# Optimization experiments

Hardware: AMD Instinct MI355X
Metric: run time of the kernel (lower is better)

Reference implementation:

```python
import jax, jax.numpy as jnp
import numpy as np

D_MODEL = 1024
N_HEAD = 16
D_K = 64
D_V = 64
LN_EPS = 1e-5


def setup_inputs() -> dict:
    key = jax.random.key(0)
    ks = jax.random.split(key, 12)
    B, S = 4, 2048
    s = 1.0 / np.sqrt(D_MODEL)
    inp = {
        "q": jax.random.normal(ks[0], (B, S, D_MODEL), jnp.float32),
        "k": jax.random.normal(ks[1], (B, S, D_MODEL), jnp.float32),
        "v": jax.random.normal(ks[2], (B, S, D_MODEL), jnp.float32),
        "mask": jnp.ones((B, S, S), jnp.int32),
        "w_q": jax.random.normal(ks[3], (D_MODEL, N_HEAD * D_K), jnp.float32) * s,
        "b_q": jnp.zeros((N_HEAD * D_K,), jnp.float32),
        "w_k": jax.random.normal(ks[4], (D_MODEL, N_HEAD * D_K), jnp.float32) * s,
        "b_k": jnp.zeros((N_HEAD * D_K,), jnp.float32),
        "w_v": jax.random.normal(ks[5], (D_MODEL, N_HEAD * D_V), jnp.float32) * s,
        "b_v": jnp.zeros((N_HEAD * D_V,), jnp.float32),
        "w_fc": jax.random.normal(ks[6], (N_HEAD * D_V, D_MODEL), jnp.float32) * s,
        "b_fc": jnp.zeros((D_MODEL,), jnp.float32),
        "ln_g": jnp.ones((D_MODEL,), jnp.float32),
        "ln_b": jnp.zeros((D_MODEL,), jnp.float32),
    }
    return inp


def reference(q, k, v, mask, w_q, b_q, w_k, b_k, w_v, b_v, w_fc, b_fc, ln_g, ln_b):
    B, Sq, _ = q.shape
    Sk = k.shape[1]
    residual = q
    # QKV projections -> [B, H, S, d]
    qh = (q @ w_q + b_q).reshape(B, Sq, N_HEAD, D_K).transpose(0, 2, 1, 3)
    kh = (k @ w_k + b_k).reshape(B, Sk, N_HEAD, D_K).transpose(0, 2, 1, 3)
    vh = (v @ w_v + b_v).reshape(B, Sk, N_HEAD, D_V).transpose(0, 2, 1, 3)
    temp = jnp.sqrt(jnp.asarray(D_K, qh.dtype))
    scores = jnp.einsum("bhqd,bhkd->bhqk", qh / temp, kh)
    scores = jnp.where(mask[:, None, :, :] == 0, jnp.asarray(-1e9, scores.dtype), scores)
    attn = jax.nn.softmax(scores, axis=-1)  # dropout is identity in eval
    out = jnp.einsum("bhqk,bhkd->bhqd", attn, vh)
    out = out.transpose(0, 2, 1, 3).reshape(B, Sq, N_HEAD * D_V)
    out = out @ w_fc + b_fc  # output proj (dropout identity)
    x = out + residual
    mu = jnp.mean(x, axis=-1, keepdims=True)
    var = jnp.mean(jnp.square(x - mu), axis=-1, keepdims=True)
    y = (x - mu) * jax.lax.rsqrt(var + LN_EPS) * ln_g + ln_b
    return (y, attn)
```

## Files before the change

### kernel.cpp

```cpp
#include <hip/hip_runtime.h>
#include <cstdint>
#include <cstddef>

#define DM 1024
#define HN 16
#define DH 64
#define BB 4
#define SS 2048
#define MM (BB * SS)

typedef __bf16 bf16;
typedef bf16 bf16x8 __attribute__((ext_vector_type(8)));
typedef bf16 bf16x4 __attribute__((ext_vector_type(4)));
typedef float f32x4 __attribute__((ext_vector_type(4)));

__device__ __forceinline__ f32x4 mfma16(bf16x8 a, bf16x8 b, f32x4 c) {
  return __builtin_amdgcn_mfma_f32_16x16x32_bf16(a, b, c, 0, 0, 0);
}

typedef __attribute__((address_space(3))) void lds_void_t;
typedef __attribute__((address_space(1))) void glob_void_t;

__device__ __forceinline__ void gload16(const void* g, void* l) {
  __builtin_amdgcn_global_load_lds((const glob_void_t*)g, (lds_void_t*)l, 16, 0, 0);
}

__global__ __launch_bounds__(256) void mask_bits(const int* __restrict__ mask,
                                                 unsigned long long* __restrict__ mbits) {
  size_t i = (size_t)blockIdx.x * 256 + threadIdx.x;
  int m = mask[i];
  unsigned long long w = __ballot(m != 0);
  if ((threadIdx.x & 63) == 0) mbits[i >> 6] = w;
}

__global__ __launch_bounds__(256) void cvt3(const float* __restrict__ q,
                                            const float* __restrict__ k,
                                            const float* __restrict__ v,
                                            bf16* __restrict__ dst) {
  int which = blockIdx.y;
  const float* in = which == 0 ? q : which == 1 ? k : v;
  bf16* out = dst + (size_t)which * MM * DM;
  int i = (blockIdx.x * 256 + threadIdx.x) * 8;
  f32x4 a = *(const f32x4*)(in + i);
  f32x4 b = *(const f32x4*)(in + i + 4);
  bf16x8 o;
  o[0] = (bf16)a[0]; o[1] = (bf16)a[1]; o[2] = (bf16)a[2]; o[3] = (bf16)a[3];
  o[4] = (bf16)b[0]; o[5] = (bf16)b[1]; o[6] = (bf16)b[2]; o[7] = (bf16)b[3];
  *(bf16x8*)(out + i) = o;
}

__global__ __launch_bounds__(256) void wtrans4(const float* __restrict__ w_q,
                                               const float* __restrict__ w_k,
                                               const float* __restrict__ w_v,
                                               const float* __restrict__ w_fc,
                                               bf16* __restrict__ WT) {
  int p = blockIdx.z;
  const float* W = p == 0 ? w_q : p == 1 ? w_k : p == 2 ? w_v : w_fc;
  bf16* out = WT + (size_t)p * DM * DM;
  __shared__ float t[32][33];
  int n0 = blockIdx.x * 32, k0 = blockIdx.y * 32;
  int tid = threadIdx.x;
  int r = tid >> 3, c = (tid & 7) * 4;
  f32x4 v = *(const f32x4*)&W[(size_t)(k0 + r) * DM + n0 + c];
  t[r][c] = v[0]; t[r][c + 1] = v[1]; t[r][c + 2] = v[2]; t[r][c + 3] = v[3];
  __syncthreads();
  bf16x4 o;
#pragma unroll
  for (int i = 0; i < 4; ++i) o[i] = (bf16)t[c + i][r];
  *(bf16x4*)&out[(size_t)(n0 + r) * DM + k0 + c] = o;
}

__global__ __launch_bounds__(256) void gemm_qkv(const bf16* __restrict__ Abase,
                                                const bf16* __restrict__ Bt,
                                                const float* __restrict__ b_q,
                                                const float* __restrict__ b_k,
                                                const float* __restrict__ b_v,
                                                bf16* __restrict__ qhh,
                                                bf16* __restrict__ khh,
                                                bf16* __restrict__ vhT) {
  constexpr int K = DM;
  __shared__ bf16 Ab[128 * 32];
  __shared__ bf16 Bb[128 * 32];
  int tid = threadIdx.x, wave = tid >> 6, lane = tid & 63;
  int bm = blockIdx.x * 128, bn = blockIdx.y * 128;
  int proj = bn >> 10;
  const bf16* A = Abase + (size_t)proj * MM * DM;
  const float* bias = proj == 0 ? b_q : proj == 1 ? b_k : b_v;
  int wr = (wave >> 1) * 64, wc = (wave & 1) * 64;
  int fr = lane & 15, kg8 = (lane >> 4) * 8;
  f32x4 acc[4][4] = {};
  int arow = tid >> 2, acol = (tid & 3) * 8;
  const bf16* Ag0 = A + (size_t)(bm + arow) * K + acol;
  const bf16* Ag1 = Ag0 + (size_t)64 * K;
  const bf16* Bg0 = Bt + (size_t)(bn + arow) * K + acol;
  const bf16* Bg1 = Bg0 + (size_t)64 * K;
  char* la = (char*)Ab + wave * 1024;
  char* lb = (char*)Bb + wave * 1024;
  for (int k0 = 0; k0 < K; k0 += 32) {
    __syncthreads();
    gload16(Ag0 + k0, la);
    gload16(Ag1 + k0, la + 4096);
    gload16(Bg0 + k0, lb);
    gload16(Bg1 + k0, lb + 4096);
    asm volatile("s_waitcnt vmcnt(0)" ::: "memory");
    __syncthreads();
    bf16x8 af[4], bfr[4];
#pragma unroll
    for (int m = 0; m < 4; ++m)
      af[m] = *(const bf16x8*)&Ab[(wr + m * 16 + fr) * 32 + kg8];
#pragma unroll
    for (int n = 0; n < 4; ++n)
      bfr[n] = *(const bf16x8*)&Bb[(wc + n * 16 + fr) * 32 + kg8];
#pragma unroll
    for (int m = 0; m < 4; ++m)
#pragma unroll
      for (int n = 0; n < 4; ++n) acc[m][n] = mfma16(af[m], bfr[n], acc[m][n]);
  }
  int b = bm >> 11;
#pragma unroll
  for (int m = 0; m < 4; ++m)
#pragma unroll
    for (int n = 0; n < 4; ++n) {
      int c = bn + wc + n * 16 + fr;
      int lc = c & 1023;
      float bv = bias[lc];
      int h = lc >> 6, d = lc & 63;
      int r0 = bm + wr + m * 16 + (lane >> 4) * 4;
      int s0 = r0 & (SS - 1);
      if (proj == 2) {
        bf16x4 o;
#pragma unroll
        for (int j = 0; j < 4; ++j) o[j] = (bf16)(acc[m][n][j] + bv);
        *(bf16x4*)&vhT[(size_t)(b * HN + h) * (SS * DH) +
                       (size_t)(s0 >> 5) * (DH * 32) + d * 32 + (s0 & 31)] = o;
      } else {
        bf16* dst = proj == 0 ? qhh : khh;
        float sc = proj == 0 ? 0.125f : 1.f;
#pragma unroll
        for (int j = 0; j < 4; ++j) {
          float v = (acc[m][n][j] + bv) * sc;
          dst[(size_t)(b * HN + h) * (SS * DH) + (size_t)(s0 + j) * DH + d] =
              (bf16)v;
        }
      }
    }
}

__global__ __launch_bounds__(256) void gemm_out(const bf16* __restrict__ A,
                                                const bf16* __restrict__ Bt,
                                                const float* __restrict__ bias,
                                                const float* __restrict__ resid,
                                                float* __restrict__ out) {
  constexpr int K = DM;
  __shared__ bf16 Ab[128 * 32];
  __shared__ bf16 Bb[128 * 32];
  int tid = threadIdx.x, wave = tid >> 6, lane = tid & 63;
  int bm = blockIdx.x * 128, bn = blockIdx.y * 128;
  int wr = (wave >> 1) * 64, wc = (wave & 1) * 64;
  int fr = lane & 15, kg8 = (lane >> 4) * 8;
  f32x4 acc[4][4] = {};
  int arow = tid >> 2, acol = (tid & 3) * 8;
  const bf16* Ag0 = A + (size_t)(bm + arow) * K + acol;
  const bf16* Ag1 = Ag0 + (size_t)64 * K;
  const bf16* Bg0 = Bt + (size_t)(bn + arow) * K + acol;
  const bf16* Bg1 = Bg0 + (size_t)64 * K;
  char* la = (char*)Ab + wave * 1024;
  char* lb = (char*)Bb + wave * 1024;
  for (int k0 = 0; k0 < K; k0 += 32) {
    __syncthreads();
    gload16(Ag0 + k0, la);
    gload16(Ag1 + k0, la + 4096);
    gload16(Bg0 + k0, lb);
    gload16(Bg1 + k0, lb + 4096);
    asm volatile("s_waitcnt vmcnt(0)" ::: "memory");
    __syncthreads();
    bf16x8 af[4], bfr[4];
#pragma unroll
    for (int m = 0; m < 4; ++m)
      af[m] = *(const bf16x8*)&Ab[(wr + m * 16 + fr) * 32 + kg8];
#pragma unroll
    for (int n = 0; n < 4; ++n)
      bfr[n] = *(const bf16x8*)&Bb[(wc + n * 16 + fr) * 32 + kg8];
#pragma unroll
    for (int m = 0; m < 4; ++m)
#pragma unroll
      for (int n = 0; n < 4; ++n) acc[m][n] = mfma16(af[m], bfr[n], acc[m][n]);
  }
#pragma unroll
  for (int m = 0; m < 4; ++m)
#pragma unroll
    for (int n = 0; n < 4; ++n) {
      int c = bn + wc + n * 16 + fr;
      float bv = bias[c];
#pragma unroll
      for (int j = 0; j < 4; ++j) {
        int r = bm + wr + m * 16 + (lane >> 4) * 4 + j;
        size_t idx = (size_t)r * DM + c;
        out[idx] = acc[m][n][j] + bv + resid[idx];
      }
    }
}

__global__ __launch_bounds__(1024, 4) void attn_kernel(
    const bf16* __restrict__ qh, const bf16* __restrict__ kh,
    const bf16* __restrict__ vhT, const unsigned int* __restrict__ mbits,
    float* __restrict__ attn_out, bf16* __restrict__ ctx) {
  extern __shared__ char smem[];
  float* pbuf = (float*)(smem + 32 * 4096);
  float* invp = (float*)(smem + 32 * 4096 + 8192);
  int tid = threadIdx.x, wave = tid >> 6, lane = tid & 63;
  int fid = (blockIdx.x & 7) * 512 + (blockIdx.x >> 3);
  int bh = fid >> 6, qt = fid & 63;
  int b = bh >> 4, h = bh & 15;
  int q0 = qt * 32;
  const bf16* qbase = qh + ((size_t)bh * SS + q0) * DH;
  const bf16* kbase = kh + (size_t)bh * SS * DH;
  const bf16* vbase = vhT + (size_t)bh * SS * DH;
  int fr = lane & 15, kg = lane >> 4;

  bf16x8 qa0 = *(const bf16x8*)&qbase[(size_t)fr * DH + kg * 8];
  bf16x8 qa1 = *(const bf16x8*)&qbase[(size_t)fr * DH + 32 + kg * 8];
  bf16x8 qb0 = *(const bf16x8*)&qbase[(size_t)(16 + fr) * DH + kg * 8];
  bf16x8 qb1 = *(const bf16x8*)&qbase[(size_t)(16 + fr) * DH + 32 + kg * 8];

  {
    int sw = wave * 128;
    bf16x8 kb0[8], kb1[8];
    auto kload = [&](int g) {
      const bf16* kp = kbase + (size_t)(sw + g * 16 + fr) * DH + kg * 8;
      kb0[g & 7] = *(const bf16x8*)kp;
      kb1[g & 7] = *(const bf16x8*)(kp + 32);
    };
#pragma unroll
    for (int g = 0; g < 4; ++g) kload(g);
#pragma unroll
    for (int g = 0; g < 8; ++g) {
      if (g < 4) kload(g + 4);
      f32x4 aa = {0.f, 0.f, 0.f, 0.f};
      f32x4 ab = {0.f, 0.f, 0.f, 0.f};
      aa = mfma16(qa0, kb0[g & 7], aa);
      aa = mfma16(qa1, kb1[g & 7], aa);
      ab = mfma16(qb0, kb0[g & 7], ab);
      ab = mfma16(qb1, kb1[g & 7], ab);
      int col = sw + g * 16 + fr;
      int slot = col >> 3, within = col & 7;
#pragma unroll
      for (int j = 0; j < 4; ++j) {
        int ra = kg * 4 + j;
        int rb = ra + 16;
        *(bf16*)(smem + ra * 4096 + ((slot ^ ra) << 4) + within * 2) =
            (bf16)aa[j];
        *(bf16*)(smem + rb * 4096 + ((slot ^ rb) << 4) + within * 2) =
            (bf16)ab[j];
      }
    }
  }
  __syncthreads();

  {
    int row = wave * 2 + (lane >> 5);
    int la = lane & 31;
    char* rbase = smem + row * 4096;
    const unsigned int* mrow32 = mbits + ((size_t)b * SS + q0 + row) * 64;
    float sum = 0.f;
#pragma unroll
    for (int it = 0; it < 8; ++it) {
      int slot = la + it * 32;
      char* p = rbase + ((slot ^ row) << 4);
      bf16x8 e = *(const bf16x8*)p;
      unsigned int bits = mrow32[slot >> 2] >> ((slot & 3) * 8);
      bf16x8 w8;
#pragma unroll
      for (int i = 0; i < 8; ++i) {
        float f = __expf((float)e[i]);
        f = ((bits >> i) & 1u) ? f : 0.f;
        sum += f;
        w8[i] = (bf16)f;
      }
      *(bf16x8*)p = w8;
    }
#pragma unroll
    for (int off = 1; off < 32; off <<= 1) sum += __shfl_xor(sum, off);
    if (la == 0) invp[row] = 1.f / sum;
  }
  __syncthreads();

  {
    int t = tid & 511, rh = tid >> 9;
    int slot = t >> 1, halfoff = (t & 1) * 8;
    float* outb = attn_out + ((size_t)bh * SS + q0) * SS;
#pragma unroll
    for (int it = 0; it < 16; ++it) {
      int r = it * 2 + rh;
      bf16x4 e = *(const bf16x4*)(smem + r * 4096 + ((slot ^ r) << 4) + halfoff);
      float inv = invp[r];
      f32x4 u = {(float)e[0] * inv, (float)e[1] * inv, (float)e[2] * inv,
                 (float)e[3] * inv};
      *(f32x4*)(outb + (size_t)r * SS + t * 4) = u;
    }
  }

  {
    int rb = wave >> 3, dq = (wave >> 1) & 3, kh2 = wave & 1;
    f32x4 cacc = {0.f, 0.f, 0.f, 0.f};
    const bf16* vtile = vbase + (size_t)(kh2 * 32) * (DH * 32) +
                        (dq * 16 + fr) * 32 + kg * 8;
    int prow_row = rb * 16 + fr;
    char* prow = smem + prow_row * 4096;
    bf16x8 vb[8], pb[8];
    auto pvload = [&](int kk) {
      vb[kk & 7] = *(const bf16x8*)&vtile[(size_t)kk * (DH * 32)];
      int slotA = kh2 * 128 + kk * 4 + kg;
      pb[kk & 7] = *(const bf16x8*)(prow + ((slotA ^ prow_row) << 4));
    };
    pvload(0);
    pvload(1);
    pvload(2);
    pvload(3);
#pragma unroll
    for (int kk = 0; kk < 32; ++kk) {
      if (kk < 28) pvload(kk + 4);
      cacc = mfma16(pb[kk & 7], vb[kk & 7], cacc);
    }
    if (kh2 == 1) {
#pragma unroll
      for (int j = 0; j < 4; ++j)
        pbuf[((rb * 4 + dq) * 16 + kg * 4 + j) * 16 + fr] = cacc[j];
    }
    __syncthreads();
    if (kh2 == 0) {
#pragma unroll
      for (int j = 0; j < 4; ++j) {
        int row = rb * 16 + kg * 4 + j;
        float v = (cacc[j] + pbuf[((rb * 4 + dq) * 16 + kg * 4 + j) * 16 + fr]) *
                  invp[row];
        ctx[((size_t)b * SS + q0 + row) * DM + h * DH + dq * 16 + fr] = (bf16)v;
      }
    }
  }
}

__global__ __launch_bounds__(256) void ln_k(float* __restrict__ x,
                                            const float* __restrict__ g,
                                            const float* __restrict__ bln) {
  int r = blockIdx.x, tid = threadIdx.x;
  f32x4 v = *(const f32x4*)&x[(size_t)r * DM + tid * 4];
  float s = v[0] + v[1] + v[2] + v[3];
  float s2 = v[0] * v[0] + v[1] * v[1] + v[2] * v[2] + v[3] * v[3];
#pragma unroll
  for (int off = 32; off; off >>= 1) {
    s += __shfl_down(s, off);
    s2 += __shfl_down(s2, off);
  }
  __shared__ float rs_[4], rs2_[4];
  int wave = tid >> 6, lane = tid & 63;
  if (lane == 0) {
    rs_[wave] = s;
    rs2_[wave] = s2;
  }
  __syncthreads();
  s = rs_[0] + rs_[1] + rs_[2] + rs_[3];
  s2 = rs2_[0] + rs2_[1] + rs2_[2] + rs2_[3];
  float mu = s * (1.f / DM);
  float var = s2 * (1.f / DM) - mu * mu;
  float rstd = rsqrtf(var + 1e-5f);
  f32x4 gg = *(const f32x4*)&g[tid * 4];
  f32x4 bb = *(const f32x4*)&bln[tid * 4];
  f32x4 o;
#pragma unroll
  for (int i = 0; i < 4; ++i) o[i] = (v[i] - mu) * rstd * gg[i] + bb[i];
  *(f32x4*)&x[(size_t)r * DM + tid * 4] = o;
}

extern "C" void kernel_launch(void* const* d_in, const int* in_sizes, int n_in,
                              void* d_out, int out_size, void* d_ws,
                              size_t ws_size, hipStream_t stream) {
  const float* q = (const float*)d_in[0];
  const float* k = (const float*)d_in[1];
  const float* v = (const float*)d_in[2];
  const int* mask = (const int*)d_in[3];
  const float* w_q = (const float*)d_in[4];
  const float* b_q = (const float*)d_in[5];
  const float* w_k = (const float*)d_in[6];
  const float* b_k = (const float*)d_in[7];
  const float* w_v = (const float*)d_in[8];
  const float* b_v = (const float*)d_in[9];
  const float* w_fc = (const float*)d_in[10];
  const float* b_fc = (const float*)d_in[11];
  const float* ln_g = (const float*)d_in[12];
  const float* ln_b = (const float*)d_in[13];

  float* y = (float*)d_out;
  float* attn_out = (float*)d_out + (size_t)MM * DM;

  char* w = (char*)d_ws;
  const size_t actN = (size_t)MM * DM;
  bf16* qkv_bf = (bf16*)w;  w += 3 * actN * 2;
  bf16* wT = (bf16*)w;      w += (size_t)4 * DM * DM * 2;
  bf16* qhh = (bf16*)w;     w += actN * 2;
  bf16* khh = (bf16*)w;     w += actN * 2;
  bf16* vhT = (bf16*)w;     w += actN * 2;
  bf16* ctx = (bf16*)w;     w += actN * 2;
  unsigned long long* mb = (unsigned long long*)w;  w += (size_t)BB * SS * SS / 8;

  mask_bits<<<(BB * SS * SS) / 256, 256, 0, stream>>>(mask, mb);
  cvt3<<<dim3(4096, 3), 256, 0, stream>>>(q, k, v, qkv_bf);
  wtrans4<<<dim3(DM / 32, DM / 32, 4), 256, 0, stream>>>(w_q, w_k, w_v, w_fc, wT);
  gemm_qkv<<<dim3(MM / 128, 3072 / 128), 256, 0, stream>>>(
      qkv_bf, wT, b_q, b_k, b_v, qhh, khh, vhT);
  hipFuncSetAttribute((const void*)attn_kernel,
                      hipFuncAttributeMaxDynamicSharedMemorySize, 139392);
  attn_kernel<<<4096, 1024, 139392, stream>>>(
      qhh, khh, vhT, (const unsigned int*)mb, attn_out, ctx);
  gemm_out<<<dim3(MM / 128, DM / 128), 256, 0, stream>>>(
      ctx, wT + (size_t)3 * DM * DM, b_fc, q, y);
  ln_k<<<MM, 256, 0, stream>>>(y, ln_g, ln_b);
}
```

Before: 671.1 us.

## Fuse exp and mask into score epilogue, transpose mask bits, move attn store last

The mask is repacked into a column-major bitmask (one 32-bit word per key column per 32-query tile), so the QK^T epilogue can apply exp and the mask directly from registers before writing to LDS. The softmax pass then only sums the row, with no read-modify-write of LDS. The full attention-probability store is moved after the PV product, so that store can overlap or trail the matmul work. The new mask kernel has each thread loop over 32 rows with strided loads, which may coalesce less well than the old ballot-based packer.

```diff
diff --git a/kernel.cpp b/kernel.cpp
--- a/kernel.cpp
+++ b/kernel.cpp
@@ -13,6 +13,7 @@
 typedef bf16 bf16x8 __attribute__((ext_vector_type(8)));
 typedef bf16 bf16x4 __attribute__((ext_vector_type(4)));
 typedef float f32x4 __attribute__((ext_vector_type(4)));
+typedef int i32x4 __attribute__((ext_vector_type(4)));
 
 __device__ __forceinline__ f32x4 mfma16(bf16x8 a, bf16x8 b, f32x4 c) {
   return __builtin_amdgcn_mfma_f32_16x16x32_bf16(a, b, c, 0, 0, 0);
@@ -25,12 +26,24 @@
   __builtin_amdgcn_global_load_lds((const glob_void_t*)g, (lds_void_t*)l, 16, 0, 0);
 }
 
-__global__ __launch_bounds__(256) void mask_bits(const int* __restrict__ mask,
-                                                 unsigned long long* __restrict__ mbits) {
-  size_t i = (size_t)blockIdx.x * 256 + threadIdx.x;
-  int m = mask[i];
-  unsigned long long w = __ballot(m != 0);
-  if ((threadIdx.x & 63) == 0) mbits[i >> 6] = w;
+__global__ __launch_bounds__(256) void mask_bitsT(const int* __restrict__ mask,
+                                                  unsigned int* __restrict__ mT) {
+  int qt = blockIdx.x, b = blockIdx.y;
+  int col0 = threadIdx.x * 8;
+  unsigned int m[8] = {0, 0, 0, 0, 0, 0, 0, 0};
+  const int* mp = mask + ((size_t)b * SS + qt * 32) * SS + col0;
+  for (int r = 0; r < 32; ++r) {
+    i32x4 a = *(const i32x4*)(mp + (size_t)r * SS);
+    i32x4 c = *(const i32x4*)(mp + (size_t)r * SS + 4);
+#pragma unroll
+    for (int i = 0; i < 4; ++i) {
+      m[i] |= (unsigned int)(a[i] != 0) << r;
+      m[4 + i] |= (unsigned int)(c[i] != 0) << r;
+    }
+  }
+#pragma unroll
+  for (int i = 0; i < 8; ++i)
+    mT[((size_t)b * 64 + qt) * SS + col0 + i] = m[i];
 }
 
 __global__ __launch_bounds__(256) void cvt3(const float* __restrict__ q,
@@ -203,7 +216,7 @@
 
 __global__ __launch_bounds__(1024, 4) void attn_kernel(
     const bf16* __restrict__ qh, const bf16* __restrict__ kh,
-    const bf16* __restrict__ vhT, const unsigned int* __restrict__ mbits,
+    const bf16* __restrict__ vhT, const unsigned int* __restrict__ mT,
     float* __restrict__ attn_out, bf16* __restrict__ ctx) {
   extern __shared__ char smem[];
   float* pbuf = (float*)(smem + 32 * 4096);
@@ -216,6 +229,7 @@
   const bf16* qbase = qh + ((size_t)bh * SS + q0) * DH;
   const bf16* kbase = kh + (size_t)bh * SS * DH;
   const bf16* vbase = vhT + (size_t)bh * SS * DH;
+  const unsigned int* mTb = mT + ((size_t)b * 64 + qt) * SS;
   int fr = lane & 15, kg = lane >> 4;
 
   bf16x8 qa0 = *(const bf16x8*)&qbase[(size_t)fr * DH + kg * 8];
@@ -243,15 +257,16 @@
       ab = mfma16(qb0, kb0[g & 7], ab);
       ab = mfma16(qb1, kb1[g & 7], ab);
       int col = sw + g * 16 + fr;
+      unsigned int bits = mTb[col];
       int slot = col >> 3, within = col & 7;
 #pragma unroll
       for (int j = 0; j < 4; ++j) {
         int ra = kg * 4 + j;
         int rb = ra + 16;
-        *(bf16*)(smem + ra * 4096 + ((slot ^ ra) << 4) + within * 2) =
-            (bf16)aa[j];
-        *(bf16*)(smem + rb * 4096 + ((slot ^ rb) << 4) + within * 2) =
-            (bf16)ab[j];
+        float fa = ((bits >> ra) & 1u) ? __expf(aa[j]) : 0.f;
+        float fb = ((bits >> rb) & 1u) ? __expf(ab[j]) : 0.f;
+        *(bf16*)(smem + ra * 4096 + ((slot ^ ra) << 4) + within * 2) = (bf16)fa;
+        *(bf16*)(smem + rb * 4096 + ((slot ^ rb) << 4) + within * 2) = (bf16)fb;
       }
     }
   }
@@ -261,44 +276,19 @@
     int row = wave * 2 + (lane >> 5);
     int la = lane & 31;
     char* rbase = smem + row * 4096;
-    const unsigned int* mrow32 = mbits + ((size_t)b * SS + q0 + row) * 64;
     float sum = 0.f;
 #pragma unroll
     for (int it = 0; it < 8; ++it) {
       int slot = la + it * 32;
-      char* p = rbase + ((slot ^ row) << 4);
-      bf16x8 e = *(const bf16x8*)p;
-      unsigned int bits = mrow32[slot >> 2] >> ((slot & 3) * 8);
-      bf16x8 w8;
-#pragma unroll
-      for (int i = 0; i < 8; ++i) {
-        float f = __expf((float)e[i]);
-        f = ((bits >> i) & 1u) ? f : 0.f;
-        sum += f;
-        w8[i] = (bf16)f;
-      }
-      *(bf16x8*)p = w8;
+      bf16x8 e = *(const bf16x8*)(rbase + ((slot ^ row) << 4));
+#pragma unroll
+      for (int i = 0; i < 8; ++i) sum += (float)e[i];
     }
 #pragma unroll
     for (int off = 1; off < 32; off <<= 1) sum += __shfl_xor(sum, off);
     if (la == 0) invp[row] = 1.f / sum;
   }
   __syncthreads();
-
-  {
-    int t = tid & 511, rh = tid >> 9;
-    int slot = t >> 1, halfoff = (t & 1) * 8;
-    float* outb = attn_out + ((size_t)bh * SS + q0) * SS;
-#pragma unroll
-    for (int it = 0; it < 16; ++it) {
-      int r = it * 2 + rh;
-      bf16x4 e = *(const bf16x4*)(smem + r * 4096 + ((slot ^ r) << 4) + halfoff);
-      float inv = invp[r];
-      f32x4 u = {(float)e[0] * inv, (float)e[1] * inv, (float)e[2] * inv,
-                 (float)e[3] * inv};
-      *(f32x4*)(outb + (size_t)r * SS + t * 4) = u;
-    }
-  }
 
   {
     int rb = wave >> 3, dq = (wave >> 1) & 3, kh2 = wave & 1;
@@ -338,6 +328,21 @@
       }
     }
   }
+
+  {
+    int t = tid & 511, rh = tid >> 9;
+    int slot = t >> 1, halfoff = (t & 1) * 8;
+    float* outb = attn_out + ((size_t)bh * SS + q0) * SS;
+#pragma unroll
+    for (int it = 0; it < 16; ++it) {
+      int r = it * 2 + rh;
+      bf16x4 e = *(const bf16x4*)(smem + r * 4096 + ((slot ^ r) << 4) + halfoff);
+      float inv = invp[r];
+      f32x4 u = {(float)e[0] * inv, (float)e[1] * inv, (float)e[2] * inv,
+                 (float)e[3] * inv};
+      *(f32x4*)(outb + (size_t)r * SS + t * 4) = u;
+    }
+  }
 }
 
 __global__ __launch_bounds__(256) void ln_k(float* __restrict__ x,
@@ -401,9 +406,9 @@
   bf16* khh = (bf16*)w;     w += actN * 2;
   bf16* vhT = (bf16*)w;     w += actN * 2;
   bf16* ctx = (bf16*)w;     w += actN * 2;
-  unsigned long long* mb = (unsigned long long*)w;  w += (size_t)BB * SS * SS / 8;
-
-  mask_bits<<<(BB * SS * SS) / 256, 256, 0, stream>>>(mask, mb);
+  unsigned int* mT = (unsigned int*)w;  w += (size_t)BB * 64 * SS * 4;
+
+  mask_bitsT<<<dim3(SS / 32, BB), 256, 0, stream>>>(mask, mT);
   cvt3<<<dim3(4096, 3), 256, 0, stream>>>(q, k, v, qkv_bf);
   wtrans4<<<dim3(DM / 32, DM / 32, 4), 256, 0, stream>>>(w_q, w_k, w_v, w_fc, wT);
   gemm_qkv<<<dim3(MM / 128, 3072 / 128), 256, 0, stream>>>(
@@ -411,7 +416,7 @@
   hipFuncSetAttribute((const void*)attn_kernel,
                       hipFuncAttributeMaxDynamicSharedMemorySize, 139392);
   attn_kernel<<<4096, 1024, 139392, stream>>>(
-      qhh, khh, vhT, (const unsigned int*)mb, attn_out, ctx);
+      qhh, khh, vhT, mT, attn_out, ctx);
   gemm_out<<<dim3(MM / 128, DM / 128), 256, 0, stream>>>(
       ctx, wT + (size_t)3 * DM * DM, b_fc, q, y);
   ln_k<<<MM, 256, 0, stream>>>(y, ln_g, ln_b);
```

New measurement: 667.2 us. No clear change (-0.6%).
